# Kernel optimization log

Hardware: AMD Instinct MI355X
Metric: run time of the kernel (lower is better)

## Reference

```python
import jax, jax.numpy as jnp
import numpy as np

DIM = 512
NUM_HEADS = 8
NUM_BLOCKS = 16
# NOTE: original code computes head_dim from FULL dim (before the reduce layer),
# so scale = (dim // num_heads) ** -0.5 = 64 ** -0.5, even though the actual
# per-head dim after reduce is 32. We preserve this quirk faithfully.
SCALE = (DIM // NUM_HEADS) ** -0.5


def setup_inputs() -> dict:
    key = jax.random.key(0)
    ks = jax.random.split(key, 5)
    B, N = 4, 4096
    C = DIM // 2
    x = jax.random.normal(ks[0], (B, N, DIM), dtype=jnp.float32)
    reduce_w = jax.random.normal(ks[1], (DIM, C), dtype=jnp.float32) * (DIM ** -0.5)
    qkv_w = jax.random.normal(ks[2], (C, 3 * C), dtype=jnp.float32) * (C ** -0.5)
    proj_w = jax.random.normal(ks[3], (C, DIM), dtype=jnp.float32) * (C ** -0.5)
    proj_b = jnp.zeros((DIM,), dtype=jnp.float32)
    return {"x": x, "reduce_w": reduce_w, "qkv_w": qkv_w,
            "proj_w": proj_w, "proj_b": proj_b}


def reference(x, reduce_w, qkv_w, proj_w, proj_b):
    B, N, _ = x.shape
    xr = x @ reduce_w                      # [B, N, C]  (C = dim/2)
    C = xr.shape[-1]
    H = NUM_HEADS
    d = C // H
    qkv = (xr @ qkv_w).reshape(B, N, 3, H, d).transpose(2, 0, 3, 1, 4)  # [3,B,H,N,d]
    q, k, v = qkv[0], qkv[1], qkv[2]
    bs = N // NUM_BLOCKS                   # block (chunk) size
    # block-diagonal local attention: reshape seq into independent blocks
    qb = q.reshape(B, H, NUM_BLOCKS, bs, d)
    kb = k.reshape(B, H, NUM_BLOCKS, bs, d)
    vb = v.reshape(B, H, NUM_BLOCKS, bs, d)
    attn = jnp.einsum('bhnqd,bhnkd->bhnqk', qb, kb) * SCALE
    attn = jax.nn.softmax(attn, axis=-1)
    ob = jnp.einsum('bhnqk,bhnkd->bhnqd', attn, vb)   # [B,H,Nb,bs,d]
    # torch: per-block transpose(1,2) then cat on dim=1 -> [B, N, H, d]
    o = ob.transpose(0, 2, 3, 1, 4).reshape(B, N, C)
    return o @ proj_w + proj_b
```

## Files before the change

kernel.cpp:

```cpp
#include <hip/hip_runtime.h>
#include <hip/hip_fp16.h>

typedef _Float16 half_t;
typedef _Float16 f16x8 __attribute__((ext_vector_type(8)));
typedef __fp16 fp16x2 __attribute__((ext_vector_type(2)));
typedef float f32x4 __attribute__((ext_vector_type(4)));

#define MFMA_F16(a, b, c) __builtin_amdgcn_mfma_f32_16x16x32_f16((a), (b), (c), 0, 0, 0)

static __device__ inline unsigned pkrtz(float a, float b) {
    union { fp16x2 h; unsigned u; } c;
    c.h = __builtin_amdgcn_cvt_pkrtz(a, b);
    return c.u;
}

__device__ __forceinline__ void gload16(const half_t* g, half_t* l) {
    __builtin_amdgcn_global_load_lds(
        (const __attribute__((address_space(1))) void*)g,
        (__attribute__((address_space(3))) void*)l, 16, 0, 0);
}

__global__ __launch_bounds__(256) void prep(
    const float* __restrict__ x, const float* __restrict__ qw,
    const float* __restrict__ rw, const float* __restrict__ pw,
    half_t* __restrict__ x_h, half_t* __restrict__ pw_t, half_t* __restrict__ Wt) {
    __shared__ __align__(16) char smem[24576];
    const int bid = blockIdx.x, tid = threadIdx.x;

    if (bid < 48) {
        char* As = smem;
        char* Bs = smem + 8192;
        const int M0 = (bid % 12) * 64, N0 = (bid / 12) * 128;
        const int lane = tid & 63, w = tid >> 6;
        const int l15 = lane & 15, l4 = lane >> 4;
        const int wrow = (w >> 1) * 32, wcol = (w & 1) * 64;
        const int pa = (l15 & 7) << 4;

        f32x4 acc[2][4];
#pragma unroll
        for (int i = 0; i < 2; ++i)
#pragma unroll
            for (int j = 0; j < 4; ++j) acc[i][j] = (f32x4){0.f, 0.f, 0.f, 0.f};

        for (int kc = 0; kc < 4; ++kc) {
            int c0 = kc * 64;
            __syncthreads();
#pragma unroll
            for (int i = 0; i < 2; ++i) {
                int j = tid + i * 256;
                int row = j >> 3, e8 = (j & 7) * 8;
                float s = (M0 + row) < 256 ? 0.125f : 1.f;
                f16x8 v;
#pragma unroll
                for (int e = 0; e < 8; ++e)
                    v[e] = (half_t)(qw[(size_t)(c0 + e8 + e) * 768 + M0 + row] * s);
                *(f16x8*)(As + row * 128 + ((e8 * 2) ^ ((row & 7) << 4))) = v;
            }
#pragma unroll
            for (int i = 0; i < 4; ++i) {
                int j = tid + i * 256;
                int row = j >> 3, e8 = (j & 7) * 8;
                const float* p = rw + (size_t)(N0 + row) * 256 + c0 + e8;
                float4 u0 = *(const float4*)p;
                float4 u1 = *(const float4*)(p + 4);
                f16x8 v;
                v[0] = (half_t)u0.x; v[1] = (half_t)u0.y;
                v[2] = (half_t)u0.z; v[3] = (half_t)u0.w;
                v[4] = (half_t)u1.x; v[5] = (half_t)u1.y;
                v[6] = (half_t)u1.z; v[7] = (half_t)u1.w;
                *(f16x8*)(Bs + row * 128 + ((e8 * 2) ^ ((row & 7) << 4))) = v;
            }
            __syncthreads();
#pragma unroll
            for (int ki = 0; ki < 2; ++ki) {
                f16x8 af[2], bf[4];
#pragma unroll
                for (int mi = 0; mi < 2; ++mi) {
                    int row = wrow + mi * 16 + l15;
                    af[mi] = *(const f16x8*)(As + row * 128 + (((ki * 4 + l4) << 4) ^ pa));
                }
#pragma unroll
                for (int nj = 0; nj < 4; ++nj) {
                    int row = wcol + nj * 16 + l15;
                    bf[nj] = *(const f16x8*)(Bs + row * 128 + (((ki * 4 + l4) << 4) ^ pa));
                }
#pragma unroll
                for (int mi = 0; mi < 2; ++mi)
#pragma unroll
                    for (int nj = 0; nj < 4; ++nj)
                        acc[mi][nj] = MFMA_F16(af[mi], bf[nj], acc[mi][nj]);
            }
        }
#pragma unroll
        for (int mi = 0; mi < 2; ++mi)
#pragma unroll
            for (int nj = 0; nj < 4; ++nj)
#pragma unroll
                for (int reg = 0; reg < 4; ++reg) {
                    int grow = M0 + wrow + mi * 16 + l4 * 4 + reg;
                    int gcol = N0 + wcol + nj * 16 + l15;
                    Wt[(size_t)grow * 512 + gcol] = (half_t)acc[mi][nj][reg];
                }
        return;
    }

    if (bid < 80) {
        half_t* tile = (half_t*)smem;
        int t = bid - 48;
        int R0 = (t >> 3) * 64, C0 = (t & 7) * 64;
#pragma unroll
        for (int e = 0; e < 16; ++e) {
            int idx = tid + e * 256;
            int r = idx >> 6, c = idx & 63;
            tile[r * 72 + c] = (half_t)pw[(size_t)(R0 + r) * 512 + C0 + c];
        }
        __syncthreads();
#pragma unroll
        for (int e = 0; e < 16; ++e) {
            int idx = tid + e * 256;
            int c = idx >> 6, r = idx & 63;
            pw_t[(size_t)(C0 + c) * 256 + R0 + r] = tile[r * 72 + c];
        }
        return;
    }

    int i8 = ((bid - 80) * 256 + tid) * 8;
    float4 a = *(const float4*)(x + i8);
    float4 b = *(const float4*)(x + i8 + 4);
    f16x8 v;
    v[0] = (half_t)a.x; v[1] = (half_t)a.y; v[2] = (half_t)a.z; v[3] = (half_t)a.w;
    v[4] = (half_t)b.x; v[5] = (half_t)b.y; v[6] = (half_t)b.z; v[7] = (half_t)b.w;
    *(f16x8*)(x_h + i8) = v;
}

template <int EPI, int K, int NB>
__global__ __launch_bounds__(256) void gemm_f16(
    const half_t* __restrict__ A, const half_t* __restrict__ Bt,
    void* __restrict__ Dst, const float* __restrict__ bias) {
    constexpr int nkt = K >> 6;
    constexpr int NLB = NB / 32;
    constexpr int NJ = NB / 32;
    constexpr int BUFSZ = 16384 + NB * 128;
    __shared__ __align__(16) char smem[2 * BUFSZ];

    const int tid = threadIdx.x;
    const int lane = tid & 63, w = tid >> 6;
    const int l15 = lane & 15, l4 = lane >> 4;
    const int wrow = (w >> 1) * 64, wcol = (w & 1) * (NB / 2);
    const int bm0 = blockIdx.x * 128;
    const int bn0 = blockIdx.y * NB;

    const half_t* srcA[4];
#pragma unroll
    for (int i = 0; i < 4; ++i) {
        int J = w * 256 + i * 64 + lane;
        int row = J >> 3, c = (J & 7) ^ (row & 7);
        srcA[i] = A + (size_t)(bm0 + row) * K + c * 8;
    }
    const half_t* srcB[NLB];
#pragma unroll
    for (int i = 0; i < NLB; ++i) {
        int J = w * (64 * NLB) + i * 64 + lane;
        int row = J >> 3, c = (J & 7) ^ (row & 7);
        srcB[i] = Bt + (size_t)(bn0 + row) * K + c * 8;
    }

    auto STAGE = [&](int kt) {
        char* As = smem + (kt & 1) * BUFSZ;
        char* Bs = As + 16384;
#pragma unroll
        for (int i = 0; i < 4; ++i)
            gload16(srcA[i] + kt * 64, (half_t*)(As + (w * 4 + i) * 1024));
#pragma unroll
        for (int i = 0; i < NLB; ++i)
            gload16(srcB[i] + kt * 64, (half_t*)(Bs + (w * NLB + i) * 1024));
    };

    f32x4 acc[4][NJ];
#pragma unroll
    for (int i = 0; i < 4; ++i)
#pragma unroll
        for (int j = 0; j < NJ; ++j) acc[i][j] = (f32x4){0.f, 0.f, 0.f, 0.f};

    const int pa = (l15 & 7) << 4;

    STAGE(0);
#pragma unroll
    for (int kt = 0; kt < nkt; ++kt) {
        if (kt + 1 < nkt) {
            STAGE(kt + 1);
            asm volatile("s_waitcnt vmcnt(%0)" ::"i"(4 + NLB) : "memory");
        } else {
            asm volatile("s_waitcnt vmcnt(0)" ::: "memory");
        }
        __builtin_amdgcn_s_barrier();
        __builtin_amdgcn_sched_barrier(0);

        const char* As = smem + (kt & 1) * BUFSZ;
        const char* Bs = As + 16384;
#pragma unroll
        for (int ki = 0; ki < 2; ++ki) {
            f16x8 af[4], bf[NJ];
#pragma unroll
            for (int mi = 0; mi < 4; ++mi) {
                int row = wrow + mi * 16 + l15;
                af[mi] = *(const f16x8*)(As + row * 128 + (((ki * 4 + l4) << 4) ^ pa));
            }
#pragma unroll
            for (int nj = 0; nj < NJ; ++nj) {
                int row = wcol + nj * 16 + l15;
                bf[nj] = *(const f16x8*)(Bs + row * 128 + (((ki * 4 + l4) << 4) ^ pa));
            }
#pragma unroll
            for (int mi = 0; mi < 4; ++mi)
#pragma unroll
                for (int nj = 0; nj < NJ; ++nj)
                    acc[mi][nj] = MFMA_F16(af[mi], bf[nj], acc[mi][nj]);
        }
        __builtin_amdgcn_sched_barrier(0);
        __builtin_amdgcn_s_barrier();
    }

#pragma unroll
    for (int mi = 0; mi < 4; ++mi) {
#pragma unroll
        for (int nj = 0; nj < NJ; ++nj) {
#pragma unroll
            for (int reg = 0; reg < 4; ++reg) {
                int grow = bm0 + wrow + mi * 16 + l4 * 4 + reg;
                int gcol = bn0 + wcol + nj * 16 + l15;
                float val = acc[mi][nj][reg];
                if (EPI == 1) {
                    int t = gcol >> 8, h = (gcol >> 5) & 7, dd = gcol & 31;
                    int b = grow >> 12, n = grow & 4095;
                    int blk = n >> 8, r = n & 255;
                    size_t base = (size_t)t * 4194304 +
                                  (size_t)((((b << 3) + h) << 4) + blk) * 8192;
                    size_t idx = (t == 2) ? base + (size_t)dd * 256 + r
                                          : base + (size_t)r * 32 + dd;
                    ((half_t*)Dst)[idx] = (half_t)val;
                } else {
                    ((float*)Dst)[(size_t)grow * 512 + gcol] = val + bias[gcol];
                }
            }
        }
    }
}

__global__ __launch_bounds__(512, 4) void attn_f16(const half_t* __restrict__ qkv_ws,
                                                   half_t* __restrict__ o_ws) {
    const int blkid = blockIdx.x;
    const int b = blkid >> 7, h = (blkid >> 4) & 7, blk = blkid & 15;
    const half_t* Q  = qkv_ws + (size_t)blkid * 8192;
    const half_t* Kp = qkv_ws + 4194304 + (size_t)blkid * 8192;
    const half_t* VT = qkv_ws + 8388608 + (size_t)blkid * 8192;

    const int tid = threadIdx.x, lane = tid & 63, w = tid >> 6;
    const int l15 = lane & 15, l4 = lane >> 4;
    const int qb = w * 32;

    f16x8 aq[2];
    aq[0] = *(const f16x8*)(Q + (qb + l15) * 32 + l4 * 8);
    aq[1] = *(const f16x8*)(Q + (qb + 16 + l15) * 32 + l4 * 8);

    float s_run[2] = {0.f, 0.f};
    f32x4 acc_o[2][2];
#pragma unroll
    for (int qg = 0; qg < 2; ++qg)
#pragma unroll
        for (int fo = 0; fo < 2; ++fo) acc_o[qg][fo] = (f32x4){0.f, 0.f, 0.f, 0.f};
    const f32x4 zero4 = (f32x4){0.f, 0.f, 0.f, 0.f};

    for (int kt = 0; kt < 4; ++kt) {
        f16x8 ka[4];
#pragma unroll
        for (int t = 0; t < 4; ++t)
            ka[t] = *(const f16x8*)(Kp + (kt * 64 + t * 16 + l15) * 32 + l4 * 8);
        f16x8 bv[2][2];
#pragma unroll
        for (int c = 0; c < 2; ++c)
#pragma unroll
            for (int fo = 0; fo < 2; ++fo)
                bv[c][fo] = *(const f16x8*)(VT + (fo * 16 + l15) * 256 + kt * 64 + c * 32 + l4 * 8);

        f32x4 st[2][4];
        __builtin_amdgcn_s_setprio(1);
#pragma unroll
        for (int qg = 0; qg < 2; ++qg)
#pragma unroll
            for (int t = 0; t < 4; ++t) st[qg][t] = MFMA_F16(ka[t], aq[qg], zero4);
        __builtin_amdgcn_s_setprio(0);

#pragma unroll
        for (int qg = 0; qg < 2; ++qg) {
            float p[4][4];
            float ps = 0.f;
#pragma unroll
            for (int t = 0; t < 4; ++t)
#pragma unroll
                for (int r = 0; r < 4; ++r) {
                    float e = __expf(st[qg][t][r]);
                    p[t][r] = e;
                    ps += e;
                }
            ps += __shfl_xor(ps, 16);
            ps += __shfl_xor(ps, 32);
            s_run[qg] += ps;

#pragma unroll
            for (int c = 0; c < 2; ++c) {
                unsigned pk0[2], pk1[2];
#pragma unroll
                for (int rp = 0; rp < 2; ++rp) {
                    pk0[rp] = pkrtz(p[2 * c][2 * rp], p[2 * c][2 * rp + 1]);
                    pk1[rp] = pkrtz(p[2 * c + 1][2 * rp], p[2 * c + 1][2 * rp + 1]);
                }
                union { unsigned u[4]; f16x8 v; } au;
#pragma unroll
                for (int j = 0; j < 4; ++j) {
                    int src = l15 + ((((l4 & 1) << 1) + (j >> 1)) << 4);
                    unsigned g0 = (unsigned)__shfl((int)pk0[j & 1], src);
                    unsigned g1 = (unsigned)__shfl((int)pk1[j & 1], src);
                    au.u[j] = (l4 < 2) ? g0 : g1;
                }
                __builtin_amdgcn_s_setprio(1);
#pragma unroll
                for (int fo = 0; fo < 2; ++fo)
                    acc_o[qg][fo] = MFMA_F16(au.v, bv[c][fo], acc_o[qg][fo]);
                __builtin_amdgcn_s_setprio(0);
            }
        }
    }

#pragma unroll
    for (int qg = 0; qg < 2; ++qg) {
        float inv = 1.f / s_run[qg];
        float sinv[4];
#pragma unroll
        for (int r = 0; r < 4; ++r) sinv[r] = __shfl(inv, (l4 << 2) | r);
#pragma unroll
        for (int fo = 0; fo < 2; ++fo)
#pragma unroll
            for (int r = 0; r < 4; ++r) {
                int grow = b * 4096 + blk * 256 + qb + qg * 16 + l4 * 4 + r;
                o_ws[(size_t)grow * 256 + h * 32 + fo * 16 + l15] =
                    (half_t)(acc_o[qg][fo][r] * sinv[r]);
            }
    }
}

extern "C" void kernel_launch(void* const* d_in, const int* in_sizes, int n_in,
                              void* d_out, int out_size, void* d_ws, size_t ws_size,
                              hipStream_t stream) {
    const float* x        = (const float*)d_in[0];
    const float* reduce_w = (const float*)d_in[1];
    const float* qkv_w    = (const float*)d_in[2];
    const float* proj_w   = (const float*)d_in[3];
    const float* proj_b   = (const float*)d_in[4];
    char* ws = (char*)d_ws;

    half_t* qkv_ws = (half_t*)ws;
    half_t* o_buf  = (half_t*)(ws + 25165824);
    half_t* pw_t   = (half_t*)(ws + 33554432);
    half_t* Wt     = (half_t*)(ws + 33816576);
    half_t* x_h    = (half_t*)(ws + 34603008);

    prep<<<4176, 256, 0, stream>>>(x, qkv_w, reduce_w, proj_w, x_h, pw_t, Wt);
    gemm_f16<1, 512, 192><<<dim3(128, 4), 256, 0, stream>>>(x_h, Wt, qkv_ws, nullptr);
    attn_f16<<<512, 512, 0, stream>>>(qkv_ws, o_buf);
    gemm_f16<2, 256, 128><<<dim3(128, 4), 256, 0, stream>>>(o_buf, pw_t, d_out, proj_b);
}
```

Baseline: 70.73 us.

## Fuse x fp32-to-fp16 conversion into QKV GEMM and fold log2e into scale

Removes the separate pass that converted x to fp16 in the prep kernel. The QKV GEMM now loads fp32 x tiles straight into LDS and packs them to fp16 in registers before the MFMA. K-steps shrink to 32 and the B tile uses a new swizzle. The query scale now includes log2(e), so attention can use exp2f instead of __expf. This saves one full write and read of the activation, at the cost of twice the LDS and global bytes per A tile and more conversion work in the GEMM inner loop.

```diff
diff --git a/kernel.cpp b/kernel.cpp
--- a/kernel.cpp
+++ b/kernel.cpp
@@ -14,16 +14,21 @@
     return c.u;
 }
 
-__device__ __forceinline__ void gload16(const half_t* g, half_t* l) {
+__device__ __forceinline__ void gload16(const half_t* g, char* l) {
     __builtin_amdgcn_global_load_lds(
         (const __attribute__((address_space(1))) void*)g,
         (__attribute__((address_space(3))) void*)l, 16, 0, 0);
 }
+__device__ __forceinline__ void gload16f(const float* g, char* l) {
+    __builtin_amdgcn_global_load_lds(
+        (const __attribute__((address_space(1))) void*)g,
+        (__attribute__((address_space(3))) void*)l, 16, 0, 0);
+}
 
 __global__ __launch_bounds__(256) void prep(
-    const float* __restrict__ x, const float* __restrict__ qw,
-    const float* __restrict__ rw, const float* __restrict__ pw,
-    half_t* __restrict__ x_h, half_t* __restrict__ pw_t, half_t* __restrict__ Wt) {
+    const float* __restrict__ qw, const float* __restrict__ rw,
+    const float* __restrict__ pw, half_t* __restrict__ pw_t,
+    half_t* __restrict__ Wt) {
     __shared__ __align__(16) char smem[24576];
     const int bid = blockIdx.x, tid = threadIdx.x;
 
@@ -49,7 +54,7 @@
             for (int i = 0; i < 2; ++i) {
                 int j = tid + i * 256;
                 int row = j >> 3, e8 = (j & 7) * 8;
-                float s = (M0 + row) < 256 ? 0.125f : 1.f;
+                float s = (M0 + row) < 256 ? 0.18033688f : 1.f;
                 f16x8 v;
 #pragma unroll
                 for (int e = 0; e < 8; ++e)
@@ -104,65 +109,50 @@
         return;
     }
 
-    if (bid < 80) {
-        half_t* tile = (half_t*)smem;
-        int t = bid - 48;
-        int R0 = (t >> 3) * 64, C0 = (t & 7) * 64;
-#pragma unroll
-        for (int e = 0; e < 16; ++e) {
-            int idx = tid + e * 256;
-            int r = idx >> 6, c = idx & 63;
-            tile[r * 72 + c] = (half_t)pw[(size_t)(R0 + r) * 512 + C0 + c];
-        }
-        __syncthreads();
-#pragma unroll
-        for (int e = 0; e < 16; ++e) {
-            int idx = tid + e * 256;
-            int c = idx >> 6, r = idx & 63;
-            pw_t[(size_t)(C0 + c) * 256 + R0 + r] = tile[r * 72 + c];
-        }
-        return;
-    }
-
-    int i8 = ((bid - 80) * 256 + tid) * 8;
-    float4 a = *(const float4*)(x + i8);
-    float4 b = *(const float4*)(x + i8 + 4);
-    f16x8 v;
-    v[0] = (half_t)a.x; v[1] = (half_t)a.y; v[2] = (half_t)a.z; v[3] = (half_t)a.w;
-    v[4] = (half_t)b.x; v[5] = (half_t)b.y; v[6] = (half_t)b.z; v[7] = (half_t)b.w;
-    *(f16x8*)(x_h + i8) = v;
-}
-
-template <int EPI, int K, int NB>
-__global__ __launch_bounds__(256) void gemm_f16(
-    const half_t* __restrict__ A, const half_t* __restrict__ Bt,
-    void* __restrict__ Dst, const float* __restrict__ bias) {
-    constexpr int nkt = K >> 6;
-    constexpr int NLB = NB / 32;
-    constexpr int NJ = NB / 32;
-    constexpr int BUFSZ = 16384 + NB * 128;
+    half_t* tile = (half_t*)smem;
+    int t = bid - 48;
+    int R0 = (t >> 3) * 64, C0 = (t & 7) * 64;
+#pragma unroll
+    for (int e = 0; e < 16; ++e) {
+        int idx = tid + e * 256;
+        int r = idx >> 6, c = idx & 63;
+        tile[r * 72 + c] = (half_t)pw[(size_t)(R0 + r) * 512 + C0 + c];
+    }
+    __syncthreads();
+#pragma unroll
+    for (int e = 0; e < 16; ++e) {
+        int idx = tid + e * 256;
+        int c = idx >> 6, r = idx & 63;
+        pw_t[(size_t)(C0 + c) * 256 + R0 + r] = tile[r * 72 + c];
+    }
+}
+
+__global__ __launch_bounds__(256) void gemm_qkv(
+    const float* __restrict__ X, const half_t* __restrict__ Bt,
+    half_t* __restrict__ Dst) {
+    constexpr int BUFSZ = 16384 + 12288;
     __shared__ __align__(16) char smem[2 * BUFSZ];
 
     const int tid = threadIdx.x;
     const int lane = tid & 63, w = tid >> 6;
     const int l15 = lane & 15, l4 = lane >> 4;
-    const int wrow = (w >> 1) * 64, wcol = (w & 1) * (NB / 2);
+    const int wrow = (w >> 1) * 64, wcol = (w & 1) * 96;
     const int bm0 = blockIdx.x * 128;
-    const int bn0 = blockIdx.y * NB;
-
-    const half_t* srcA[4];
+    const int bn0 = blockIdx.y * 192;
+
+    const float* srcA[4];
 #pragma unroll
     for (int i = 0; i < 4; ++i) {
         int J = w * 256 + i * 64 + lane;
         int row = J >> 3, c = (J & 7) ^ (row & 7);
-        srcA[i] = A + (size_t)(bm0 + row) * K + c * 8;
-    }
-    const half_t* srcB[NLB];
-#pragma unroll
-    for (int i = 0; i < NLB; ++i) {
-        int J = w * (64 * NLB) + i * 64 + lane;
-        int row = J >> 3, c = (J & 7) ^ (row & 7);
-        srcB[i] = Bt + (size_t)(bn0 + row) * K + c * 8;
+        srcA[i] = X + (size_t)(bm0 + row) * 512 + c * 4;
+    }
+    const half_t* srcB[3];
+#pragma unroll
+    for (int i = 0; i < 3; ++i) {
+        int J = w * 192 + i * 64 + lane;
+        int row = J >> 2, c = ((J & 3) - (row >> 1)) & 3;
+        srcB[i] = Bt + (size_t)(bn0 + row) * 512 + c * 8;
     }
 
     auto STAGE = [&](int kt) {
@@ -170,26 +160,24 @@
         char* Bs = As + 16384;
 #pragma unroll
         for (int i = 0; i < 4; ++i)
-            gload16(srcA[i] + kt * 64, (half_t*)(As + (w * 4 + i) * 1024));
-#pragma unroll
-        for (int i = 0; i < NLB; ++i)
-            gload16(srcB[i] + kt * 64, (half_t*)(Bs + (w * NLB + i) * 1024));
+            gload16f(srcA[i] + kt * 32, As + (w * 4 + i) * 1024);
+#pragma unroll
+        for (int i = 0; i < 3; ++i)
+            gload16(srcB[i] + kt * 32, Bs + (w * 3 + i) * 1024);
     };
 
-    f32x4 acc[4][NJ];
+    f32x4 acc[4][6];
 #pragma unroll
     for (int i = 0; i < 4; ++i)
 #pragma unroll
-        for (int j = 0; j < NJ; ++j) acc[i][j] = (f32x4){0.f, 0.f, 0.f, 0.f};
-
-    const int pa = (l15 & 7) << 4;
+        for (int j = 0; j < 6; ++j) acc[i][j] = (f32x4){0.f, 0.f, 0.f, 0.f};
 
     STAGE(0);
 #pragma unroll
-    for (int kt = 0; kt < nkt; ++kt) {
-        if (kt + 1 < nkt) {
+    for (int kt = 0; kt < 16; ++kt) {
+        if (kt + 1 < 16) {
             STAGE(kt + 1);
-            asm volatile("s_waitcnt vmcnt(%0)" ::"i"(4 + NLB) : "memory");
+            asm volatile("s_waitcnt vmcnt(7)" ::: "memory");
         } else {
             asm volatile("s_waitcnt vmcnt(0)" ::: "memory");
         }
@@ -198,25 +186,32 @@
 
         const char* As = smem + (kt & 1) * BUFSZ;
         const char* Bs = As + 16384;
-#pragma unroll
-        for (int ki = 0; ki < 2; ++ki) {
-            f16x8 af[4], bf[NJ];
-#pragma unroll
-            for (int mi = 0; mi < 4; ++mi) {
-                int row = wrow + mi * 16 + l15;
-                af[mi] = *(const f16x8*)(As + row * 128 + (((ki * 4 + l4) << 4) ^ pa));
-            }
-#pragma unroll
-            for (int nj = 0; nj < NJ; ++nj) {
-                int row = wcol + nj * 16 + l15;
-                bf[nj] = *(const f16x8*)(Bs + row * 128 + (((ki * 4 + l4) << 4) ^ pa));
-            }
-#pragma unroll
-            for (int mi = 0; mi < 4; ++mi)
-#pragma unroll
-                for (int nj = 0; nj < NJ; ++nj)
-                    acc[mi][nj] = MFMA_F16(af[mi], bf[nj], acc[mi][nj]);
-        }
+
+        f16x8 af[4], bf[6];
+#pragma unroll
+        for (int mi = 0; mi < 4; ++mi) {
+            int row = wrow + mi * 16 + l15;
+            f32x4 lo = *(const f32x4*)(As + row * 128 + (((l4 * 2) ^ (row & 7)) << 4));
+            f32x4 hi = *(const f32x4*)(As + row * 128 + (((l4 * 2 + 1) ^ (row & 7)) << 4));
+            union { unsigned u[4]; f16x8 v; } cu;
+            cu.u[0] = pkrtz(lo[0], lo[1]);
+            cu.u[1] = pkrtz(lo[2], lo[3]);
+            cu.u[2] = pkrtz(hi[0], hi[1]);
+            cu.u[3] = pkrtz(hi[2], hi[3]);
+            af[mi] = cu.v;
+        }
+#pragma unroll
+        for (int nj = 0; nj < 6; ++nj) {
+            int row = wcol + nj * 16 + l15;
+            int p = (l4 + (row >> 1)) & 3;
+            bf[nj] = *(const f16x8*)(Bs + row * 64 + p * 16);
+        }
+#pragma unroll
+        for (int mi = 0; mi < 4; ++mi)
+#pragma unroll
+            for (int nj = 0; nj < 6; ++nj)
+                acc[mi][nj] = MFMA_F16(af[mi], bf[nj], acc[mi][nj]);
+
         __builtin_amdgcn_sched_barrier(0);
         __builtin_amdgcn_s_barrier();
     }
@@ -224,27 +219,119 @@
 #pragma unroll
     for (int mi = 0; mi < 4; ++mi) {
 #pragma unroll
-        for (int nj = 0; nj < NJ; ++nj) {
+        for (int nj = 0; nj < 6; ++nj) {
 #pragma unroll
             for (int reg = 0; reg < 4; ++reg) {
                 int grow = bm0 + wrow + mi * 16 + l4 * 4 + reg;
                 int gcol = bn0 + wcol + nj * 16 + l15;
                 float val = acc[mi][nj][reg];
-                if (EPI == 1) {
-                    int t = gcol >> 8, h = (gcol >> 5) & 7, dd = gcol & 31;
-                    int b = grow >> 12, n = grow & 4095;
-                    int blk = n >> 8, r = n & 255;
-                    size_t base = (size_t)t * 4194304 +
-                                  (size_t)((((b << 3) + h) << 4) + blk) * 8192;
-                    size_t idx = (t == 2) ? base + (size_t)dd * 256 + r
-                                          : base + (size_t)r * 32 + dd;
-                    ((half_t*)Dst)[idx] = (half_t)val;
-                } else {
-                    ((float*)Dst)[(size_t)grow * 512 + gcol] = val + bias[gcol];
-                }
-            }
-        }
-    }
+                int t = gcol >> 8, h = (gcol >> 5) & 7, dd = gcol & 31;
+                int b = grow >> 12, n = grow & 4095;
+                int blk = n >> 8, r = n & 255;
+                size_t base = (size_t)t * 4194304 +
+                              (size_t)((((b << 3) + h) << 4) + blk) * 8192;
+                size_t idx = (t == 2) ? base + (size_t)dd * 256 + r
+                                      : base + (size_t)r * 32 + dd;
+                Dst[idx] = (half_t)val;
+            }
+        }
+    }
+}
+
+__global__ __launch_bounds__(256) void gemm_proj(
+    const half_t* __restrict__ A, const half_t* __restrict__ Bt,
+    float* __restrict__ Dst, const float* __restrict__ bias) {
+    constexpr int BUFSZ = 16384 + 16384;
+    __shared__ __align__(16) char smem[2 * BUFSZ];
+
+    const int tid = threadIdx.x;
+    const int lane = tid & 63, w = tid >> 6;
+    const int l15 = lane & 15, l4 = lane >> 4;
+    const int wrow = (w >> 1) * 64, wcol = (w & 1) * 64;
+    const int bm0 = blockIdx.x * 128;
+    const int bn0 = blockIdx.y * 128;
+
+    const half_t* srcA[4];
+#pragma unroll
+    for (int i = 0; i < 4; ++i) {
+        int J = w * 256 + i * 64 + lane;
+        int row = J >> 3, c = (J & 7) ^ (row & 7);
+        srcA[i] = A + (size_t)(bm0 + row) * 256 + c * 8;
+    }
+    const half_t* srcB[4];
+#pragma unroll
+    for (int i = 0; i < 4; ++i) {
+        int J = w * 256 + i * 64 + lane;
+        int row = J >> 3, c = (J & 7) ^ (row & 7);
+        srcB[i] = Bt + (size_t)(bn0 + row) * 256 + c * 8;
+    }
+
+    auto STAGE = [&](int kt) {
+        char* As = smem + (kt & 1) * BUFSZ;
+        char* Bs = As + 16384;
+#pragma unroll
+        for (int i = 0; i < 4; ++i)
+            gload16(srcA[i] + kt * 64, As + (w * 4 + i) * 1024);
+#pragma unroll
+        for (int i = 0; i < 4; ++i)
+            gload16(srcB[i] + kt * 64, Bs + (w * 4 + i) * 1024);
+    };
+
+    f32x4 acc[4][4];
+#pragma unroll
+    for (int i = 0; i < 4; ++i)
+#pragma unroll
+        for (int j = 0; j < 4; ++j) acc[i][j] = (f32x4){0.f, 0.f, 0.f, 0.f};
+
+    const int pa = (l15 & 7) << 4;
+
+    STAGE(0);
+#pragma unroll
+    for (int kt = 0; kt < 4; ++kt) {
+        if (kt + 1 < 4) {
+            STAGE(kt + 1);
+            asm volatile("s_waitcnt vmcnt(8)" ::: "memory");
+        } else {
+            asm volatile("s_waitcnt vmcnt(0)" ::: "memory");
+        }
+        __builtin_amdgcn_s_barrier();
+        __builtin_amdgcn_sched_barrier(0);
+
+        const char* As = smem + (kt & 1) * BUFSZ;
+        const char* Bs = As + 16384;
+#pragma unroll
+        for (int ki = 0; ki < 2; ++ki) {
+            f16x8 af[4], bf[4];
+#pragma unroll
+            for (int mi = 0; mi < 4; ++mi) {
+                int row = wrow + mi * 16 + l15;
+                af[mi] = *(const f16x8*)(As + row * 128 + (((ki * 4 + l4) << 4) ^ pa));
+            }
+#pragma unroll
+            for (int nj = 0; nj < 4; ++nj) {
+                int row = wcol + nj * 16 + l15;
+                bf[nj] = *(const f16x8*)(Bs + row * 128 + (((ki * 4 + l4) << 4) ^ pa));
+            }
+#pragma unroll
+            for (int mi = 0; mi < 4; ++mi)
+#pragma unroll
+                for (int nj = 0; nj < 4; ++nj)
+                    acc[mi][nj] = MFMA_F16(af[mi], bf[nj], acc[mi][nj]);
+        }
+        __builtin_amdgcn_sched_barrier(0);
+        __builtin_amdgcn_s_barrier();
+    }
+
+#pragma unroll
+    for (int mi = 0; mi < 4; ++mi)
+#pragma unroll
+        for (int nj = 0; nj < 4; ++nj)
+#pragma unroll
+            for (int reg = 0; reg < 4; ++reg) {
+                int grow = bm0 + wrow + mi * 16 + l4 * 4 + reg;
+                int gcol = bn0 + wcol + nj * 16 + l15;
+                Dst[(size_t)grow * 512 + gcol] = acc[mi][nj][reg] + bias[gcol];
+            }
 }
 
 __global__ __launch_bounds__(512, 4) void attn_f16(const half_t* __restrict__ qkv_ws,
@@ -299,7 +386,7 @@
             for (int t = 0; t < 4; ++t)
 #pragma unroll
                 for (int r = 0; r < 4; ++r) {
-                    float e = __expf(st[qg][t][r]);
+                    float e = exp2f(st[qg][t][r]);
                     p[t][r] = e;
                     ps += e;
                 }
@@ -363,10 +450,9 @@
     half_t* o_buf  = (half_t*)(ws + 25165824);
     half_t* pw_t   = (half_t*)(ws + 33554432);
     half_t* Wt     = (half_t*)(ws + 33816576);
-    half_t* x_h    = (half_t*)(ws + 34603008);
-
-    prep<<<4176, 256, 0, stream>>>(x, qkv_w, reduce_w, proj_w, x_h, pw_t, Wt);
-    gemm_f16<1, 512, 192><<<dim3(128, 4), 256, 0, stream>>>(x_h, Wt, qkv_ws, nullptr);
+
+    prep<<<80, 256, 0, stream>>>(qkv_w, reduce_w, proj_w, pw_t, Wt);
+    gemm_qkv<<<dim3(128, 4), 256, 0, stream>>>(x, Wt, qkv_ws);
     attn_f16<<<512, 512, 0, stream>>>(qkv_ws, o_buf);
-    gemm_f16<2, 256, 128><<<dim3(128, 4), 256, 0, stream>>>(o_buf, pw_t, d_out, proj_b);
-}
+    gemm_proj<<<dim3(128, 4), 256, 0, stream>>>(o_buf, pw_t, (float*)d_out, proj_b);
+}
```

Measured after the change: 71.06 us. No clear change (+0.5%).

## Fuse fp32-to-fp16 input conversion into QKV GEMM and retile GEMMs

Applied to the files above, without the earlier changes.

Drops the separate x-to-fp16 conversion pass from the prep kernel. The first GEMM now reads fp32 x directly and converts it while loading into registers, which saves writing and re-reading an fp16 copy of x. The GEMM is rewritten from double-buffered direct global-to-LDS loads to register-staged single-buffer loads with 64-row tiles and a different grid. The Q scale now folds in log2(e) so the softmax can use exp2f. The simpler pipeline and smaller tiles may lose latency hiding and increase B-tile reloads.

```diff
diff --git a/kernel.cpp b/kernel.cpp
--- a/kernel.cpp
+++ b/kernel.cpp
@@ -14,16 +14,10 @@
     return c.u;
 }
 
-__device__ __forceinline__ void gload16(const half_t* g, half_t* l) {
-    __builtin_amdgcn_global_load_lds(
-        (const __attribute__((address_space(1))) void*)g,
-        (__attribute__((address_space(3))) void*)l, 16, 0, 0);
-}
-
 __global__ __launch_bounds__(256) void prep(
-    const float* __restrict__ x, const float* __restrict__ qw,
-    const float* __restrict__ rw, const float* __restrict__ pw,
-    half_t* __restrict__ x_h, half_t* __restrict__ pw_t, half_t* __restrict__ Wt) {
+    const float* __restrict__ qw, const float* __restrict__ rw,
+    const float* __restrict__ pw, half_t* __restrict__ pw_t,
+    half_t* __restrict__ Wt) {
     __shared__ __align__(16) char smem[24576];
     const int bid = blockIdx.x, tid = threadIdx.x;
 
@@ -49,7 +43,7 @@
             for (int i = 0; i < 2; ++i) {
                 int j = tid + i * 256;
                 int row = j >> 3, e8 = (j & 7) * 8;
-                float s = (M0 + row) < 256 ? 0.125f : 1.f;
+                float s = (M0 + row) < 256 ? 0.18033688f : 1.f;
                 f16x8 v;
 #pragma unroll
                 for (int e = 0; e < 8; ++e)
@@ -104,127 +98,120 @@
         return;
     }
 
-    if (bid < 80) {
-        half_t* tile = (half_t*)smem;
-        int t = bid - 48;
-        int R0 = (t >> 3) * 64, C0 = (t & 7) * 64;
-#pragma unroll
-        for (int e = 0; e < 16; ++e) {
-            int idx = tid + e * 256;
-            int r = idx >> 6, c = idx & 63;
-            tile[r * 72 + c] = (half_t)pw[(size_t)(R0 + r) * 512 + C0 + c];
-        }
-        __syncthreads();
-#pragma unroll
-        for (int e = 0; e < 16; ++e) {
-            int idx = tid + e * 256;
-            int c = idx >> 6, r = idx & 63;
-            pw_t[(size_t)(C0 + c) * 256 + R0 + r] = tile[r * 72 + c];
-        }
-        return;
-    }
-
-    int i8 = ((bid - 80) * 256 + tid) * 8;
-    float4 a = *(const float4*)(x + i8);
-    float4 b = *(const float4*)(x + i8 + 4);
-    f16x8 v;
-    v[0] = (half_t)a.x; v[1] = (half_t)a.y; v[2] = (half_t)a.z; v[3] = (half_t)a.w;
-    v[4] = (half_t)b.x; v[5] = (half_t)b.y; v[6] = (half_t)b.z; v[7] = (half_t)b.w;
-    *(f16x8*)(x_h + i8) = v;
-}
-
-template <int EPI, int K, int NB>
+    half_t* tile = (half_t*)smem;
+    int t = bid - 48;
+    int R0 = (t >> 3) * 64, C0 = (t & 7) * 64;
+#pragma unroll
+    for (int e = 0; e < 16; ++e) {
+        int idx = tid + e * 256;
+        int r = idx >> 6, c = idx & 63;
+        tile[r * 72 + c] = (half_t)pw[(size_t)(R0 + r) * 512 + C0 + c];
+    }
+    __syncthreads();
+#pragma unroll
+    for (int e = 0; e < 16; ++e) {
+        int idx = tid + e * 256;
+        int c = idx >> 6, r = idx & 63;
+        pw_t[(size_t)(C0 + c) * 256 + R0 + r] = tile[r * 72 + c];
+    }
+}
+
+template <int EPI, bool AFP32, int NB, int K>
 __global__ __launch_bounds__(256) void gemm_f16(
-    const half_t* __restrict__ A, const half_t* __restrict__ Bt,
+    const void* __restrict__ Aop, const half_t* __restrict__ Bt,
     void* __restrict__ Dst, const float* __restrict__ bias) {
     constexpr int nkt = K >> 6;
-    constexpr int NLB = NB / 32;
-    constexpr int NJ = NB / 32;
-    constexpr int BUFSZ = 16384 + NB * 128;
-    __shared__ __align__(16) char smem[2 * BUFSZ];
+    constexpr int NBC = NB / 32;
+    __shared__ __align__(16) char smem[8192 + NB * 128];
+    char* As = smem;
+    char* Bs = smem + 8192;
 
     const int tid = threadIdx.x;
     const int lane = tid & 63, w = tid >> 6;
     const int l15 = lane & 15, l4 = lane >> 4;
-    const int wrow = (w >> 1) * 64, wcol = (w & 1) * (NB / 2);
-    const int bm0 = blockIdx.x * 128;
+    const int wrow = (w >> 1) * 32, wcol = (w & 1) * (NB / 2);
+    const int bm0 = blockIdx.x * 64;
     const int bn0 = blockIdx.y * NB;
-
-    const half_t* srcA[4];
-#pragma unroll
-    for (int i = 0; i < 4; ++i) {
-        int J = w * 256 + i * 64 + lane;
-        int row = J >> 3, c = (J & 7) ^ (row & 7);
-        srcA[i] = A + (size_t)(bm0 + row) * K + c * 8;
-    }
-    const half_t* srcB[NLB];
-#pragma unroll
-    for (int i = 0; i < NLB; ++i) {
-        int J = w * (64 * NLB) + i * 64 + lane;
-        int row = J >> 3, c = (J & 7) ^ (row & 7);
-        srcB[i] = Bt + (size_t)(bn0 + row) * K + c * 8;
-    }
-
-    auto STAGE = [&](int kt) {
-        char* As = smem + (kt & 1) * BUFSZ;
-        char* Bs = As + 16384;
-#pragma unroll
-        for (int i = 0; i < 4; ++i)
-            gload16(srcA[i] + kt * 64, (half_t*)(As + (w * 4 + i) * 1024));
-#pragma unroll
-        for (int i = 0; i < NLB; ++i)
-            gload16(srcB[i] + kt * 64, (half_t*)(Bs + (w * NLB + i) * 1024));
+    const int pa = (l15 & 7) << 4;
+
+    f32x4 acc[2][NBC];
+#pragma unroll
+    for (int i = 0; i < 2; ++i)
+#pragma unroll
+        for (int j = 0; j < NBC; ++j) acc[i][j] = (f32x4){0.f, 0.f, 0.f, 0.f};
+
+    f16x8 aReg[2], bReg[NBC];
+
+    auto load_tile = [&](int kt) {
+#pragma unroll
+        for (int i = 0; i < 2; ++i) {
+            int c = tid + i * 256;
+            int row = c >> 3, k0 = (c & 7) * 8;
+            int gk = kt * 64 + k0;
+            if (AFP32) {
+                const float* Af = (const float*)Aop + (size_t)(bm0 + row) * K + gk;
+                float4 u0 = *(const float4*)Af;
+                float4 u1 = *(const float4*)(Af + 4);
+                f16x8 v;
+                v[0] = (half_t)u0.x; v[1] = (half_t)u0.y;
+                v[2] = (half_t)u0.z; v[3] = (half_t)u0.w;
+                v[4] = (half_t)u1.x; v[5] = (half_t)u1.y;
+                v[6] = (half_t)u1.z; v[7] = (half_t)u1.w;
+                aReg[i] = v;
+            } else {
+                aReg[i] = *(const f16x8*)((const half_t*)Aop + (size_t)(bm0 + row) * K + gk);
+            }
+        }
+#pragma unroll
+        for (int i = 0; i < NBC; ++i) {
+            int c = tid + i * 256;
+            int row = c >> 3, k0 = (c & 7) * 8;
+            bReg[i] = *(const f16x8*)(Bt + (size_t)(bn0 + row) * K + kt * 64 + k0);
+        }
     };
 
-    f32x4 acc[4][NJ];
-#pragma unroll
-    for (int i = 0; i < 4; ++i)
-#pragma unroll
-        for (int j = 0; j < NJ; ++j) acc[i][j] = (f32x4){0.f, 0.f, 0.f, 0.f};
-
-    const int pa = (l15 & 7) << 4;
-
-    STAGE(0);
-#pragma unroll
+    load_tile(0);
     for (int kt = 0; kt < nkt; ++kt) {
-        if (kt + 1 < nkt) {
-            STAGE(kt + 1);
-            asm volatile("s_waitcnt vmcnt(%0)" ::"i"(4 + NLB) : "memory");
-        } else {
-            asm volatile("s_waitcnt vmcnt(0)" ::: "memory");
-        }
-        __builtin_amdgcn_s_barrier();
-        __builtin_amdgcn_sched_barrier(0);
-
-        const char* As = smem + (kt & 1) * BUFSZ;
-        const char* Bs = As + 16384;
+        __syncthreads();
+#pragma unroll
+        for (int i = 0; i < 2; ++i) {
+            int c = tid + i * 256;
+            int row = c >> 3, k0 = (c & 7) * 8;
+            *(f16x8*)(As + row * 128 + ((k0 * 2) ^ ((row & 7) << 4))) = aReg[i];
+        }
+#pragma unroll
+        for (int i = 0; i < NBC; ++i) {
+            int c = tid + i * 256;
+            int row = c >> 3, k0 = (c & 7) * 8;
+            *(f16x8*)(Bs + row * 128 + ((k0 * 2) ^ ((row & 7) << 4))) = bReg[i];
+        }
+        __syncthreads();
+        if (kt + 1 < nkt) load_tile(kt + 1);
 #pragma unroll
         for (int ki = 0; ki < 2; ++ki) {
-            f16x8 af[4], bf[NJ];
-#pragma unroll
-            for (int mi = 0; mi < 4; ++mi) {
+            f16x8 af[2], bf[NBC];
+#pragma unroll
+            for (int mi = 0; mi < 2; ++mi) {
                 int row = wrow + mi * 16 + l15;
                 af[mi] = *(const f16x8*)(As + row * 128 + (((ki * 4 + l4) << 4) ^ pa));
             }
 #pragma unroll
-            for (int nj = 0; nj < NJ; ++nj) {
+            for (int nj = 0; nj < NBC; ++nj) {
                 int row = wcol + nj * 16 + l15;
                 bf[nj] = *(const f16x8*)(Bs + row * 128 + (((ki * 4 + l4) << 4) ^ pa));
             }
 #pragma unroll
-            for (int mi = 0; mi < 4; ++mi)
-#pragma unroll
-                for (int nj = 0; nj < NJ; ++nj)
+            for (int mi = 0; mi < 2; ++mi)
+#pragma unroll
+                for (int nj = 0; nj < NBC; ++nj)
                     acc[mi][nj] = MFMA_F16(af[mi], bf[nj], acc[mi][nj]);
         }
-        __builtin_amdgcn_sched_barrier(0);
-        __builtin_amdgcn_s_barrier();
-    }
-
-#pragma unroll
-    for (int mi = 0; mi < 4; ++mi) {
-#pragma unroll
-        for (int nj = 0; nj < NJ; ++nj) {
+    }
+
+#pragma unroll
+    for (int mi = 0; mi < 2; ++mi) {
+#pragma unroll
+        for (int nj = 0; nj < NBC; ++nj) {
 #pragma unroll
             for (int reg = 0; reg < 4; ++reg) {
                 int grow = bm0 + wrow + mi * 16 + l4 * 4 + reg;
@@ -299,7 +286,7 @@
             for (int t = 0; t < 4; ++t)
 #pragma unroll
                 for (int r = 0; r < 4; ++r) {
-                    float e = __expf(st[qg][t][r]);
+                    float e = exp2f(st[qg][t][r]);
                     p[t][r] = e;
                     ps += e;
                 }
@@ -363,10 +350,9 @@
     half_t* o_buf  = (half_t*)(ws + 25165824);
     half_t* pw_t   = (half_t*)(ws + 33554432);
     half_t* Wt     = (half_t*)(ws + 33816576);
-    half_t* x_h    = (half_t*)(ws + 34603008);
-
-    prep<<<4176, 256, 0, stream>>>(x, qkv_w, reduce_w, proj_w, x_h, pw_t, Wt);
-    gemm_f16<1, 512, 192><<<dim3(128, 4), 256, 0, stream>>>(x_h, Wt, qkv_ws, nullptr);
+
+    prep<<<80, 256, 0, stream>>>(qkv_w, reduce_w, proj_w, pw_t, Wt);
+    gemm_f16<1, true, 192, 512><<<dim3(256, 4), 256, 0, stream>>>(x, Wt, qkv_ws, nullptr);
     attn_f16<<<512, 512, 0, stream>>>(qkv_ws, o_buf);
-    gemm_f16<2, 256, 128><<<dim3(128, 4), 256, 0, stream>>>(o_buf, pw_t, d_out, proj_b);
-}
+    gemm_f16<2, false, 256, 256><<<dim3(256, 2), 256, 0, stream>>>(o_buf, pw_t, d_out, proj_b);
+}
```

Result: no change. 71.69 us (+1.4%).
